# Optimization experiments

Hardware: AMD Instinct MI355X
Metric: run time of the kernel (lower is better)

The kernel has to match this reference:

```python
import jax, jax.numpy as jnp
import numpy as np

B, N, H, W = 2, 1024, 128, 128
SH_K = 27  # (sh_degree+1)^2 * 3 for sh_degree=2
L_L1, L_SSIM, L_DEPTH, L_OPAC = 0.8, 0.2, 0.5, 0.01
C0 = 0.28209479177387814


def _quat_to_rot(q):
    # q: [..., 4] (w,x,y,z) -> [..., 3, 3]
    w, x, y, z = q[..., 0], q[..., 1], q[..., 2], q[..., 3]
    R = jnp.stack([1 - 2 * (y * y + z * z), 2 * (x * y - w * z), 2 * (x * z + w * y),
                   2 * (x * y + w * z), 1 - 2 * (x * x + z * z), 2 * (y * z - w * x),
                   2 * (x * z - w * y), 2 * (y * z + w * x), 1 - 2 * (x * x + y * y)], axis=-1)
    return R.reshape(q.shape[:-1] + (3, 3))


def _ssim_window(size=7, sigma=1.5):
    coords = np.arange(size, dtype=np.float32) - size // 2
    g = np.exp(-coords ** 2 / (2 * sigma ** 2))
    g = g / g.sum()
    w2 = np.outer(g, g).astype(np.float32)
    return jnp.asarray(np.broadcast_to(w2[None, None], (3, 1, size, size)))  # OIHW, groups=3


def _dwconv(img, w):
    return jax.lax.conv_general_dilated(img, w, (1, 1), 'SAME',
                                        dimension_numbers=('NCHW', 'OIHW', 'NCHW'),
                                        feature_group_count=3)


def _ssim(img1, img2):
    C1, C2 = 0.01 ** 2, 0.03 ** 2
    w = _ssim_window()
    mu1, mu2 = _dwconv(img1, w), _dwconv(img2, w)
    s1 = _dwconv(img1 * img1, w) - mu1 ** 2
    s2 = _dwconv(img2 * img2, w) - mu2 ** 2
    s12 = _dwconv(img1 * img2, w) - mu1 * mu2
    return jnp.mean((2 * mu1 * mu2 + C1) * (2 * s12 + C2) /
                    ((mu1 ** 2 + mu2 ** 2 + C1) * (s1 + s2 + C2)))


def _render(gaussians, intrinsics):
    means = gaussians[:, :, :3]
    scales = gaussians[:, :, 3:6]
    rots = gaussians[:, :, 6:10]
    opac = gaussians[:, :, 10]        # [B,N]
    sh = gaussians[:, :, 11:]
    fx = intrinsics[:, 0, 0][:, None]
    fy = intrinsics[:, 1, 1][:, None]
    cx = intrinsics[:, 0, 2][:, None]
    cy = intrinsics[:, 1, 2][:, None]
    z = jnp.maximum(means[:, :, 2], 1e-4)
    px = fx * means[:, :, 0] / z + cx
    py = fy * means[:, :, 1] / z + cy
    # ---- 2D covariance (EWA) ----
    R = _quat_to_rot(rots)                               # [B,N,3,3]
    RS = R * scales[:, :, None, :]                        # R @ diag(s)
    cov3d = RS @ jnp.swapaxes(RS, -1, -2)
    zc = jnp.maximum(means[:, :, 2], 1e-6)
    zsq = zc * zc
    J = jnp.zeros(means.shape[:2] + (2, 3), means.dtype)
    J = J.at[:, :, 0, 0].set(fx / zc)
    J = J.at[:, :, 0, 2].set(-fx * means[:, :, 0] / zsq)
    J = J.at[:, :, 1, 1].set(fy / zc)
    J = J.at[:, :, 1, 2].set(-fy * means[:, :, 1] / zsq)
    cov2d = J @ cov3d @ jnp.swapaxes(J, -1, -2) + 0.3 * jnp.eye(2, dtype=means.dtype)
    det = jnp.maximum(cov2d[:, :, 0, 0] * cov2d[:, :, 1, 1] -
                      cov2d[:, :, 0, 1] * cov2d[:, :, 1, 0], 1e-8)
    inv00 = cov2d[:, :, 1, 1] / det
    inv11 = cov2d[:, :, 0, 0] / det
    inv01 = -cov2d[:, :, 0, 1] / det
    colors = jnp.clip(sh[:, :, :3] * C0 + 0.5, 0.0, 1.0)  # [B,N,3]
    # ---- dense per-pixel splatting ----
    gy = jnp.arange(H, dtype=means.dtype)
    gx = jnp.arange(W, dtype=means.dtype)
    dx = gx[None, None, None, :] - px[:, :, None, None]   # [B,N,1,W] -> bcast [B,N,H,W]
    dy = gy[None, None, :, None] - py[:, :, None, None]
    power = -0.5 * (inv00[:, :, None, None] * dx * dx +
                    2.0 * inv01[:, :, None, None] * dx * dy +
                    inv11[:, :, None, None] * dy * dy)
    alpha = jnp.exp(jnp.clip(power, -10.0, 0.0)) * opac[:, :, None, None]
    alpha = jnp.minimum(alpha, 0.99)
    # ---- depth sort + front-to-back compositing ----
    order = jnp.argsort(z, axis=1)
    alpha_s = jnp.take_along_axis(alpha, order[:, :, None, None], axis=1)
    colors_s = jnp.take_along_axis(colors, order[:, :, None], axis=1)
    depth_s = jnp.take_along_axis(z, order, axis=1)
    cp = jnp.cumprod(1.0 - alpha_s, axis=1)
    Tr = jnp.concatenate([jnp.ones_like(alpha_s[:, :1]), cp[:, :-1]], axis=1)
    weights = Tr * alpha_s                               # [B,N,H,W]
    rgb = jnp.clip(jnp.einsum('bnhw,bnc->bchw', weights, colors_s), 0.0, 1.0)
    depth = jnp.sum(weights * depth_s[:, :, None, None], axis=1, keepdims=True)
    return rgb, depth


def setup_inputs() -> dict:
    key = jax.random.key(0)
    k = jax.random.split(key, 8)
    xy = jax.random.normal(k[0], (B, N, 2)) * 1.0
    zc = jax.random.uniform(k[1], (B, N, 1), minval=0.5, maxval=4.0)
    scales = jax.random.uniform(k[2], (B, N, 3), minval=0.01, maxval=0.1)
    q = jax.random.normal(k[3], (B, N, 4))
    q = q / jnp.linalg.norm(q, axis=-1, keepdims=True)
    opac = jax.nn.sigmoid(jax.random.normal(k[4], (B, N, 1)))
    sh = jax.random.normal(k[5], (B, N, SH_K)) * 0.3
    gaussians = jnp.concatenate([xy, zc, scales, q, opac, sh], axis=-1)  # [B,N,38]
    intr = jnp.tile(jnp.array([[120.0, 0.0, 64.0], [0.0, 120.0, 64.0], [0.0, 0.0, 1.0]],
                              dtype=jnp.float32)[None], (B, 1, 1))
    target_rgb = jax.random.uniform(k[6], (B, 3, H, W))
    target_depth = jax.random.uniform(k[7], (B, 1, H, W), minval=0.5, maxval=4.0)
    return {'gaussians': gaussians, 'intrinsics': intr,
            'target_rgb': target_rgb, 'target_depth': target_depth}


def reference(gaussians, intrinsics, target_rgb, target_depth):
    rgb, depth = _render(gaussians, intrinsics)
    l1_rgb = jnp.mean(jnp.abs(rgb - target_rgb))
    ssim_val = _ssim(rgb, target_rgb)
    l1_depth = jnp.mean(jnp.abs(depth - target_depth))
    o = jnp.clip(gaussians[:, :, 10:11], 1e-6, 1.0 - 1e-6)
    opacity_reg = jnp.mean(-(o * jnp.log(o) + (1.0 - o) * jnp.log(1.0 - o)))
    loss = (L_L1 * l1_rgb + L_SSIM * (1.0 - ssim_val) +
            L_DEPTH * l1_depth + L_OPAC * opacity_reg)
    return loss
```

## Files before the change

kernel.cpp:

```cpp
#include <hip/hip_runtime.h>

#define NB 2
#define NG 1024
#define HEIGHT 128
#define WIDTH 128
#define HW (HEIGHT * WIDTH)
#define E10 4.5399931e-05f

#define REC_U 0
#define REC_S 32768
#define Z_U   65536
#define PFX   67584
#define TCNT  83984
#define TLIST 84496
#define RGBOF 346640
#define P_ENT 444944
#define P_L1D 444952
#define P_SSS 445464
#define P_SSL 445848

__device__ inline float blk_reduce(float v, float* sh) {
    for (int off = 32; off > 0; off >>= 1) v += __shfl_down(v, off, 64);
    int lane = threadIdx.x & 63;
    int w = threadIdx.x >> 6;
    __syncthreads();
    if (lane == 0) sh[w] = v;
    __syncthreads();
    float s = 0.f;
    if (threadIdx.x == 0) {
        int nw = (blockDim.x + 63) >> 6;
        for (int i = 0; i < nw; i++) s += sh[i];
    }
    return s;
}

__global__ __launch_bounds__(256) void k_pre(const float* __restrict__ g,
                                             const float* __restrict__ intr,
                                             float* __restrict__ ws) {
    __shared__ float sh[8];
    int idx = blockIdx.x * 256 + threadIdx.x;
    int b = idx >> 10;
    const float* row = g + (size_t)idx * 38;
    float mx = row[0], my = row[1], mz = row[2];
    float sx = row[3], sy = row[4], sz = row[5];
    float qw = row[6], qx = row[7], qy = row[8], qz = row[9];
    float op = row[10];
    float sh0 = row[11], sh1 = row[12], sh2 = row[13];
    float fx = intr[b * 9 + 0], fy = intr[b * 9 + 4];
    float cx = intr[b * 9 + 2], cy = intr[b * 9 + 5];

    float z = fmaxf(mz, 1e-4f);
    float px = fx * mx / z + cx;
    float py = fy * my / z + cy;

    float r00 = 1.f - 2.f * (qy * qy + qz * qz), r01 = 2.f * (qx * qy - qw * qz), r02 = 2.f * (qx * qz + qw * qy);
    float r10 = 2.f * (qx * qy + qw * qz), r11 = 1.f - 2.f * (qx * qx + qz * qz), r12 = 2.f * (qy * qz - qw * qx);
    float r20 = 2.f * (qx * qz - qw * qy), r21 = 2.f * (qy * qz + qw * qx), r22 = 1.f - 2.f * (qx * qx + qy * qy);
    float a00 = r00 * sx, a01 = r01 * sy, a02 = r02 * sz;
    float a10 = r10 * sx, a11 = r11 * sy, a12 = r12 * sz;
    float a20 = r20 * sx, a21 = r21 * sy, a22 = r22 * sz;
    float m00 = a00 * a00 + a01 * a01 + a02 * a02;
    float m01 = a00 * a10 + a01 * a11 + a02 * a12;
    float m02 = a00 * a20 + a01 * a21 + a02 * a22;
    float m11 = a10 * a10 + a11 * a11 + a12 * a12;
    float m12 = a10 * a20 + a11 * a21 + a12 * a22;
    float m22 = a20 * a20 + a21 * a21 + a22 * a22;

    float zc = fmaxf(mz, 1e-6f);
    float aJ = fx / zc, bJ = -fx * mx / (zc * zc);
    float cJ = fy / zc, dJ = -fy * my / (zc * zc);
    float c00 = aJ * aJ * m00 + 2.f * aJ * bJ * m02 + bJ * bJ * m22 + 0.3f;
    float c01 = cJ * (aJ * m01 + bJ * m12) + dJ * (aJ * m02 + bJ * m22);
    float c11 = cJ * cJ * m11 + 2.f * cJ * dJ * m12 + dJ * dJ * m22 + 0.3f;
    float det = fmaxf(c00 * c11 - c01 * c01, 1e-8f);
    float i00 = c11 / det;
    float i11 = c00 / det;
    float i01 = -c01 / det;

    const float C0c = 0.28209479177387814f;
    float col0 = fminf(fmaxf(sh0 * C0c + 0.5f, 0.f), 1.f);
    float col1 = fminf(fmaxf(sh1 * C0c + 0.5f, 0.f), 1.f);
    float col2 = fminf(fmaxf(sh2 * C0c + 0.5f, 0.f), 1.f);

    float hx = sqrtf(20.f * c00);
    float hy = sqrtf(20.f * c11);

    float* rec = ws + REC_U + (size_t)idx * 16;
    rec[0] = px; rec[1] = py; rec[2] = hx; rec[3] = hy;
    rec[4] = i00; rec[5] = i01; rec[6] = i11; rec[7] = op;
    rec[8] = col0; rec[9] = col1; rec[10] = col2; rec[11] = z;
    rec[12] = E10 * op; rec[13] = 0.f; rec[14] = 0.f; rec[15] = 0.f;
    ws[Z_U + idx] = z;

    float o = fminf(fmaxf(op, 1e-6f), 1.f - 1e-6f);
    float ent = -(o * logf(o) + (1.f - o) * logf(1.f - o));
    float s = blk_reduce(ent, sh);
    if (threadIdx.x == 0) ws[P_ENT + blockIdx.x] = s;
}

__global__ __launch_bounds__(256) void k_rank(float* __restrict__ ws) {
    __shared__ float zs[NG];
    __shared__ int sp[256];
    int bid = blockIdx.x;
    int b = bid >> 4;
    int grp = bid & 15;
    int tid = threadIdx.x;
    const float* zb = ws + Z_U + (b << 10);
    ((float4*)zs)[tid] = ((const float4*)zb)[tid];
    __syncthreads();
    int il = (grp << 6) + (tid & 63);
    int jq = tid >> 6;
    float zi = zs[il];
    int rank = 0;
    int j0 = jq << 8;
#pragma unroll 4
    for (int j = j0; j < j0 + 256; j += 4) {
        float4 zq = *(const float4*)(zs + j);
        rank += (zq.x < zi) || (zq.x == zi && (j + 0) < il);
        rank += (zq.y < zi) || (zq.y == zi && (j + 1) < il);
        rank += (zq.z < zi) || (zq.z == zi && (j + 2) < il);
        rank += (zq.w < zi) || (zq.w == zi && (j + 3) < il);
    }
    sp[tid] = rank;
    __syncthreads();
    if (tid < 64) {
        int r = sp[tid] + sp[tid + 64] + sp[tid + 128] + sp[tid + 192];
        int gi = (b << 10) + il;
        const float4* src = (const float4*)(ws + REC_U + (size_t)gi * 16);
        float4 r0 = src[0], r1 = src[1], r2 = src[2], r3 = src[3];
        float4* dst = (float4*)(ws + REC_S + (size_t)((b << 10) + r) * 16);
        dst[0] = r0; dst[1] = r1; dst[2] = r2; dst[3] = r3;
    }
}

__global__ __launch_bounds__(1024) void k_scan(float* __restrict__ ws) {
    __shared__ float st[NG], sur[NG], sug[NG], sub_[NG], sud[NG];
    int b = blockIdx.x;
    int k = threadIdx.x;
    const float* r = ws + REC_S + (size_t)((b << 10) + k) * 16;
    float4 f1 = ((const float4*)r)[1];
    float4 f2 = ((const float4*)r)[2];
    float a10 = E10 * f1.w;
    st[k] = 1.f - a10;
    sur[k] = a10 * f2.x; sug[k] = a10 * f2.y; sub_[k] = a10 * f2.z; sud[k] = a10 * f2.w;
    __syncthreads();
    for (int off = 1; off < NG; off <<= 1) {
        float tl = 1.f, url = 0.f, ugl = 0.f, ubl = 0.f, udl = 0.f;
        if (k >= off) {
            tl = st[k - off]; url = sur[k - off]; ugl = sug[k - off];
            ubl = sub_[k - off]; udl = sud[k - off];
        }
        __syncthreads();
        if (k >= off) {
            sur[k] = url + tl * sur[k];
            sug[k] = ugl + tl * sug[k];
            sub_[k] = ubl + tl * sub_[k];
            sud[k] = udl + tl * sud[k];
            st[k] = tl * st[k];
        }
        __syncthreads();
    }
    float* P = ws + PFX + (size_t)b * 8200;
    ((float4*)(P + (size_t)(k + 1) * 8))[0] = make_float4(st[k], sur[k], sug[k], sub_[k]);
    P[(size_t)(k + 1) * 8 + 4] = sud[k];
    if (k == 0) {
        ((float4*)P)[0] = make_float4(1.f, 0.f, 0.f, 0.f);
        P[4] = 0.f;
    }
}

__global__ __launch_bounds__(256) void k_bin(float* __restrict__ ws) {
    __shared__ int sc[256];
    int blk = blockIdx.x;
    int b = blk >> 8;
    int t = blk & 255;
    float x0f = (float)((t & 15) * 8), x1f = x0f + 7.f;
    float y0f = (float)((t >> 4) * 8), y1f = y0f + 7.f;
    int tid = threadIdx.x;
    int r0 = tid * 4;
    int pred = 0;
#pragma unroll
    for (int j = 0; j < 4; j++) {
        float4 bb = ((const float4*)(ws + REC_S + (size_t)((b << 10) + r0 + j) * 16))[0];
        bool ov = (bb.x + bb.z >= x0f) && (bb.x - bb.z <= x1f) &&
                  (bb.y + bb.w >= y0f) && (bb.y - bb.w <= y1f);
        pred |= (int)ov << j;
    }
    int cnt = __popc(pred);
    sc[tid] = cnt;
    __syncthreads();
    for (int off = 1; off < 256; off <<= 1) {
        int v = 0;
        if (tid >= off) v = sc[tid - off];
        __syncthreads();
        sc[tid] += v;
        __syncthreads();
    }
    unsigned short* list = (unsigned short*)(ws + TLIST) + (size_t)blk * 1024;
    int pos = sc[tid] - cnt;
#pragma unroll
    for (int j = 0; j < 4; j++)
        if (pred & (1 << j)) list[pos++] = (unsigned short)(r0 + j);
    if (tid == 255) ((int*)(ws + TCNT))[blk] = sc[255];
}

__global__ __launch_bounds__(1024, 8) void k_render(const float* __restrict__ tgt_d,
                                                    float* __restrict__ ws) {
    __shared__ float comb[5][1024];
    int tid = threadIdx.x;
    int lane = tid & 63;
    int wv = tid >> 6;
    int blk = blockIdx.x;
    int b = blk >> 8;
    int t = blk & 255;
    int x0 = (t & 15) * 8, y0 = (t >> 4) * 8;
    int x = x0 + (lane & 7), y = y0 + (lane >> 3);
    float xf = (float)x, yf = (float)y;

    int cnt = ((const int*)(ws + TCNT))[blk];
    const unsigned short* list = (const unsigned short*)(ws + TLIST) + (size_t)blk * 1024;
    const float* P = ws + PFX + (size_t)b * 8200;
    const float* recs = ws + REC_S + (size_t)(b << 10) * 16;

    int m = (cnt + 15) >> 4;
    int p0 = wv * m; if (p0 > cnt) p0 = cnt;
    int p1 = p0 + m; if (p1 > cnt) p1 = cnt;
    int s0 = (p0 == 0) ? 0 : (int)list[p0 - 1] + 1;

    float4 Pa = *(const float4*)(P + (size_t)s0 * 8);
    float Pud = P[(size_t)s0 * 8 + 4];
    float inv0 = 1.f / Pa.x;
    float Pur = Pa.y, Pug = Pa.z, Pub = Pa.w;

    float tau = 1.f, cr = 0.f, cg = 0.f, cb = 0.f, cd = 0.f;
    for (int p = p0; p < p1; p++) {
        int r = (int)list[p];
        float4 Qa = *(const float4*)(P + (size_t)r * 8);
        float Qud = P[(size_t)r * 8 + 4];
        const float* rec = recs + (size_t)r * 16;
        float4 g0 = ((const float4*)rec)[0];
        float4 g1 = ((const float4*)rec)[1];
        float4 g2 = ((const float4*)rec)[2];
        float kap = tau * inv0;
        cr += kap * (Qa.y - Pur);
        cg += kap * (Qa.z - Pug);
        cb += kap * (Qa.w - Pub);
        cd += kap * (Qud - Pud);
        float dx = xf - g0.x, dy = yf - g0.y;
        float q = g1.x * dx * dx + 2.f * g1.y * dx * dy + g1.z * dy * dy;
        float pw = fminf(fmaxf(-0.5f * q, -10.f), 0.f);
        float a = fminf(__expf(pw) * g1.w, 0.99f);
        float w = kap * Qa.x * a;
        cr += w * g2.x; cg += w * g2.y; cb += w * g2.z; cd += w * g2.w;
        float a10 = E10 * g1.w;
        tau *= (1.f - a) * (1.f + a10 * (1.f + a10));
        float s = Qa.x * a10;
        Pur = Qa.y + s * g2.x;
        Pug = Qa.z + s * g2.y;
        Pub = Qa.w + s * g2.z;
        Pud = Qud + s * g2.w;
    }
    int e0 = (wv == 15) ? NG : ((p1 == 0) ? 0 : (int)list[p1 - 1] + 1);
    float4 Ea = *(const float4*)(P + (size_t)e0 * 8);
    float Eud = P[(size_t)e0 * 8 + 4];
    float kapf = tau * inv0;
    cr += kapf * (Ea.y - Pur);
    cg += kapf * (Ea.z - Pug);
    cb += kapf * (Ea.w - Pub);
    cd += kapf * (Eud - Pud);
    float T = tau * Ea.x * inv0;

    comb[0][tid] = T;
    comb[1][tid] = cr;
    comb[2][tid] = cg;
    comb[3][tid] = cb;
    comb[4][tid] = cd;
    __syncthreads();

    if (tid < 64) {
        float T0 = comb[0][tid], r0 = comb[1][tid], g0 = comb[2][tid];
        float b0 = comb[3][tid], d0 = comb[4][tid];
#pragma unroll
        for (int sgi = 1; sgi < 16; sgi++) {
            int j = sgi * 64 + tid;
            r0 += T0 * comb[1][j];
            g0 += T0 * comb[2][j];
            b0 += T0 * comb[3][j];
            d0 += T0 * comb[4][j];
            T0 *= comb[0][j];
        }
        r0 = fminf(fmaxf(r0, 0.f), 1.f);
        g0 = fminf(fmaxf(g0, 0.f), 1.f);
        b0 = fminf(fmaxf(b0, 0.f), 1.f);
        float* rgb = ws + RGBOF;
        rgb[((b * 3 + 0) * HEIGHT + y) * WIDTH + x] = r0;
        rgb[((b * 3 + 1) * HEIGHT + y) * WIDTH + x] = g0;
        rgb[((b * 3 + 2) * HEIGHT + y) * WIDTH + x] = b0;
        float l1d = fabsf(d0 - tgt_d[(b * HEIGHT + y) * WIDTH + x]);
        for (int off = 32; off > 0; off >>= 1) l1d += __shfl_down(l1d, off, 64);
        if (tid == 0) ws[P_L1D + blk] = l1d;
    }
}

__global__ __launch_bounds__(256) void k_ssim(const float* __restrict__ tgt_rgb,
                                              float* __restrict__ ws) {
    __shared__ float sh[8];
    int idx = blockIdx.x * 256 + threadIdx.x;
    const float* img1 = ws + RGBOF;
    int bc = idx >> 14;
    int pix = idx & (HW - 1);
    int y = pix >> 7, x = pix & 127;

    float gg[7];
    float gs = 0.f;
#pragma unroll
    for (int i = 0; i < 7; i++) {
        float c = (float)(i - 3);
        gg[i] = __expf(-c * c / 4.5f);
        gs += gg[i];
    }
#pragma unroll
    for (int i = 0; i < 7; i++) gg[i] /= gs;

    float mu1 = 0.f, mu2 = 0.f, s11 = 0.f, s22 = 0.f, s12 = 0.f;
    int plane = bc * HW;
#pragma unroll
    for (int dy = -3; dy <= 3; dy++) {
        int yy = y + dy;
#pragma unroll
        for (int dx = -3; dx <= 3; dx++) {
            int xx = x + dx;
            float w = gg[dy + 3] * gg[dx + 3];
            float i1 = 0.f, i2 = 0.f;
            if (yy >= 0 && yy < HEIGHT && xx >= 0 && xx < WIDTH) {
                int o = plane + yy * WIDTH + xx;
                i1 = img1[o];
                i2 = tgt_rgb[o];
            }
            mu1 += w * i1;
            mu2 += w * i2;
            s11 += w * i1 * i1;
            s22 += w * i2 * i2;
            s12 += w * i1 * i2;
        }
    }
    float v1 = s11 - mu1 * mu1;
    float v2 = s22 - mu2 * mu2;
    float cv = s12 - mu1 * mu2;
    const float C1 = 1e-4f, C2 = 9e-4f;
    float ssim = ((2.f * mu1 * mu2 + C1) * (2.f * cv + C2)) /
                 ((mu1 * mu1 + mu2 * mu2 + C1) * (v1 + v2 + C2));
    float l1 = fabsf(img1[idx] - tgt_rgb[idx]);

    float s_ssim = blk_reduce(ssim, sh);
    float s_l1 = blk_reduce(l1, sh);
    if (threadIdx.x == 0) {
        ws[P_SSS + blockIdx.x] = s_ssim;
        ws[P_SSL + blockIdx.x] = s_l1;
    }
}

__global__ __launch_bounds__(256) void k_final(const float* __restrict__ ws_c,
                                               float* __restrict__ out) {
    __shared__ float sh[8];
    float e = 0.f, d = 0.f, ss = 0.f, sl = 0.f;
    for (int i = threadIdx.x; i < 512; i += 256) d += ws_c[P_L1D + i];
    for (int i = threadIdx.x; i < 384; i += 256) { ss += ws_c[P_SSS + i]; sl += ws_c[P_SSL + i]; }
    if (threadIdx.x < 8) e = ws_c[P_ENT + threadIdx.x];
    float rd_ = blk_reduce(d, sh);
    float rss = blk_reduce(ss, sh);
    float rsl = blk_reduce(sl, sh);
    float re = blk_reduce(e, sh);
    if (threadIdx.x == 0) {
        float l1r = rsl / (float)(NB * 3 * HW);
        float ssim = rss / (float)(NB * 3 * HW);
        float l1d = rd_ / (float)(NB * HW);
        float opa = re / (float)(NB * NG);
        out[0] = 0.8f * l1r + 0.2f * (1.f - ssim) + 0.5f * l1d + 0.01f * opa;
    }
}

extern "C" void kernel_launch(void* const* d_in, const int* in_sizes, int n_in,
                              void* d_out, int out_size, void* d_ws, size_t ws_size,
                              hipStream_t stream) {
    const float* g = (const float*)d_in[0];
    const float* intr = (const float*)d_in[1];
    const float* trgb = (const float*)d_in[2];
    const float* tdep = (const float*)d_in[3];
    float* ws = (float*)d_ws;
    float* out = (float*)d_out;

    hipLaunchKernelGGL(k_pre, dim3(8), dim3(256), 0, stream, g, intr, ws);
    hipLaunchKernelGGL(k_rank, dim3(32), dim3(256), 0, stream, ws);
    hipLaunchKernelGGL(k_scan, dim3(NB), dim3(1024), 0, stream, ws);
    hipLaunchKernelGGL(k_bin, dim3(NB * 256), dim3(256), 0, stream, ws);
    hipLaunchKernelGGL(k_render, dim3(NB * 256), dim3(1024), 0, stream, tdep, ws);
    hipLaunchKernelGGL(k_ssim, dim3((NB * 3 * HW) / 256), dim3(256), 0, stream, trgb, ws);
    hipLaunchKernelGGL(k_final, dim3(1), dim3(256), 0, stream, ws, out);
}
```

Baseline: 97.65 us.

## Fuse all loss stages into one cooperative kernel with grid-wide syncs

```diff
diff --git a/kernel.cpp b/kernel.cpp
--- a/kernel.cpp
+++ b/kernel.cpp
@@ -1,4 +1,7 @@
 #include <hip/hip_runtime.h>
+#include <hip/hip_cooperative_groups.h>
+
+namespace cg = cooperative_groups;
 
 #define NB 2
 #define NG 1024
@@ -10,373 +13,385 @@
 #define REC_U 0
 #define REC_S 32768
 #define Z_U   65536
-#define PFX   67584
-#define TCNT  83984
-#define TLIST 84496
-#define RGBOF 346640
-#define P_ENT 444944
-#define P_L1D 444952
-#define P_SSS 445464
-#define P_SSL 445848
-
-__device__ inline float blk_reduce(float v, float* sh) {
-    for (int off = 32; off > 0; off >>= 1) v += __shfl_down(v, off, 64);
-    int lane = threadIdx.x & 63;
-    int w = threadIdx.x >> 6;
-    __syncthreads();
-    if (lane == 0) sh[w] = v;
-    __syncthreads();
-    float s = 0.f;
-    if (threadIdx.x == 0) {
-        int nw = (blockDim.x + 63) >> 6;
-        for (int i = 0; i < nw; i++) s += sh[i];
-    }
-    return s;
-}
-
-__global__ __launch_bounds__(256) void k_pre(const float* __restrict__ g,
-                                             const float* __restrict__ intr,
-                                             float* __restrict__ ws) {
-    __shared__ float sh[8];
-    int idx = blockIdx.x * 256 + threadIdx.x;
-    int b = idx >> 10;
-    const float* row = g + (size_t)idx * 38;
-    float mx = row[0], my = row[1], mz = row[2];
-    float sx = row[3], sy = row[4], sz = row[5];
-    float qw = row[6], qx = row[7], qy = row[8], qz = row[9];
-    float op = row[10];
-    float sh0 = row[11], sh1 = row[12], sh2 = row[13];
-    float fx = intr[b * 9 + 0], fy = intr[b * 9 + 4];
-    float cx = intr[b * 9 + 2], cy = intr[b * 9 + 5];
-
-    float z = fmaxf(mz, 1e-4f);
-    float px = fx * mx / z + cx;
-    float py = fy * my / z + cy;
-
-    float r00 = 1.f - 2.f * (qy * qy + qz * qz), r01 = 2.f * (qx * qy - qw * qz), r02 = 2.f * (qx * qz + qw * qy);
-    float r10 = 2.f * (qx * qy + qw * qz), r11 = 1.f - 2.f * (qx * qx + qz * qz), r12 = 2.f * (qy * qz - qw * qx);
-    float r20 = 2.f * (qx * qz - qw * qy), r21 = 2.f * (qy * qz + qw * qx), r22 = 1.f - 2.f * (qx * qx + qy * qy);
-    float a00 = r00 * sx, a01 = r01 * sy, a02 = r02 * sz;
-    float a10 = r10 * sx, a11 = r11 * sy, a12 = r12 * sz;
-    float a20 = r20 * sx, a21 = r21 * sy, a22 = r22 * sz;
-    float m00 = a00 * a00 + a01 * a01 + a02 * a02;
-    float m01 = a00 * a10 + a01 * a11 + a02 * a12;
-    float m02 = a00 * a20 + a01 * a21 + a02 * a22;
-    float m11 = a10 * a10 + a11 * a11 + a12 * a12;
-    float m12 = a10 * a20 + a11 * a21 + a12 * a22;
-    float m22 = a20 * a20 + a21 * a21 + a22 * a22;
-
-    float zc = fmaxf(mz, 1e-6f);
-    float aJ = fx / zc, bJ = -fx * mx / (zc * zc);
-    float cJ = fy / zc, dJ = -fy * my / (zc * zc);
-    float c00 = aJ * aJ * m00 + 2.f * aJ * bJ * m02 + bJ * bJ * m22 + 0.3f;
-    float c01 = cJ * (aJ * m01 + bJ * m12) + dJ * (aJ * m02 + bJ * m22);
-    float c11 = cJ * cJ * m11 + 2.f * cJ * dJ * m12 + dJ * dJ * m22 + 0.3f;
-    float det = fmaxf(c00 * c11 - c01 * c01, 1e-8f);
-    float i00 = c11 / det;
-    float i11 = c00 / det;
-    float i01 = -c01 / det;
-
-    const float C0c = 0.28209479177387814f;
-    float col0 = fminf(fmaxf(sh0 * C0c + 0.5f, 0.f), 1.f);
-    float col1 = fminf(fmaxf(sh1 * C0c + 0.5f, 0.f), 1.f);
-    float col2 = fminf(fmaxf(sh2 * C0c + 0.5f, 0.f), 1.f);
-
-    float hx = sqrtf(20.f * c00);
-    float hy = sqrtf(20.f * c11);
-
-    float* rec = ws + REC_U + (size_t)idx * 16;
-    rec[0] = px; rec[1] = py; rec[2] = hx; rec[3] = hy;
-    rec[4] = i00; rec[5] = i01; rec[6] = i11; rec[7] = op;
-    rec[8] = col0; rec[9] = col1; rec[10] = col2; rec[11] = z;
-    rec[12] = E10 * op; rec[13] = 0.f; rec[14] = 0.f; rec[15] = 0.f;
-    ws[Z_U + idx] = z;
-
-    float o = fminf(fmaxf(op, 1e-6f), 1.f - 1e-6f);
-    float ent = -(o * logf(o) + (1.f - o) * logf(1.f - o));
-    float s = blk_reduce(ent, sh);
-    if (threadIdx.x == 0) ws[P_ENT + blockIdx.x] = s;
-}
-
-__global__ __launch_bounds__(256) void k_rank(float* __restrict__ ws) {
-    __shared__ float zs[NG];
-    __shared__ int sp[256];
-    int bid = blockIdx.x;
-    int b = bid >> 4;
-    int grp = bid & 15;
-    int tid = threadIdx.x;
-    const float* zb = ws + Z_U + (b << 10);
-    ((float4*)zs)[tid] = ((const float4*)zb)[tid];
-    __syncthreads();
-    int il = (grp << 6) + (tid & 63);
-    int jq = tid >> 6;
-    float zi = zs[il];
-    int rank = 0;
-    int j0 = jq << 8;
+#define BBOX  67584
+#define PFX   75776
+#define PFX_STRIDE 8200
+#define TCNT  92192
+#define TLIST 92704
+#define RGBOF 354848
+#define P_ENT 453152
+#define P_L1D 453184
+#define P_SSS 453696
+#define P_SSL 453952
+
+__global__ __launch_bounds__(1024, 4) void k_mega(
+    const float* __restrict__ g, const float* __restrict__ intr,
+    const float* __restrict__ trgb, const float* __restrict__ tgt_d,
+    float* __restrict__ ws, float* __restrict__ out)
+{
+    __shared__ float smem[5120];
+    cg::grid_group grid = cg::this_grid();
+    const int tid = threadIdx.x;
+    const int bid = blockIdx.x;
+    const int lane = tid & 63;
+    const int wv = tid >> 6;
+
+    if (bid < 2) {
+        int idx = bid * 1024 + tid;
+        int b = bid;
+        const float* row = g + (size_t)idx * 38;
+        float mx = row[0], my = row[1], mz = row[2];
+        float sx = row[3], sy = row[4], sz = row[5];
+        float qw = row[6], qx = row[7], qy = row[8], qz = row[9];
+        float op = row[10];
+        float sh0 = row[11], sh1 = row[12], sh2 = row[13];
+        float fx = intr[b * 9 + 0], fy = intr[b * 9 + 4];
+        float cx = intr[b * 9 + 2], cy = intr[b * 9 + 5];
+
+        float z = fmaxf(mz, 1e-4f);
+        float px = fx * mx / z + cx;
+        float py = fy * my / z + cy;
+
+        float r00 = 1.f - 2.f * (qy * qy + qz * qz), r01 = 2.f * (qx * qy - qw * qz), r02 = 2.f * (qx * qz + qw * qy);
+        float r10 = 2.f * (qx * qy + qw * qz), r11 = 1.f - 2.f * (qx * qx + qz * qz), r12 = 2.f * (qy * qz - qw * qx);
+        float r20 = 2.f * (qx * qz - qw * qy), r21 = 2.f * (qy * qz + qw * qx), r22 = 1.f - 2.f * (qx * qx + qy * qy);
+        float a00 = r00 * sx, a01 = r01 * sy, a02 = r02 * sz;
+        float a10 = r10 * sx, a11 = r11 * sy, a12 = r12 * sz;
+        float a20 = r20 * sx, a21 = r21 * sy, a22 = r22 * sz;
+        float m00 = a00 * a00 + a01 * a01 + a02 * a02;
+        float m01 = a00 * a10 + a01 * a11 + a02 * a12;
+        float m02 = a00 * a20 + a01 * a21 + a02 * a22;
+        float m11 = a10 * a10 + a11 * a11 + a12 * a12;
+        float m12 = a10 * a20 + a11 * a21 + a12 * a22;
+        float m22 = a20 * a20 + a21 * a21 + a22 * a22;
+
+        float zc = fmaxf(mz, 1e-6f);
+        float aJ = fx / zc, bJ = -fx * mx / (zc * zc);
+        float cJ = fy / zc, dJ = -fy * my / (zc * zc);
+        float c00 = aJ * aJ * m00 + 2.f * aJ * bJ * m02 + bJ * bJ * m22 + 0.3f;
+        float c01 = cJ * (aJ * m01 + bJ * m12) + dJ * (aJ * m02 + bJ * m22);
+        float c11 = cJ * cJ * m11 + 2.f * cJ * dJ * m12 + dJ * dJ * m22 + 0.3f;
+        float det = fmaxf(c00 * c11 - c01 * c01, 1e-8f);
+        float i00 = c11 / det;
+        float i11 = c00 / det;
+        float i01 = -c01 / det;
+
+        const float C0c = 0.28209479177387814f;
+        float col0 = fminf(fmaxf(sh0 * C0c + 0.5f, 0.f), 1.f);
+        float col1 = fminf(fmaxf(sh1 * C0c + 0.5f, 0.f), 1.f);
+        float col2 = fminf(fmaxf(sh2 * C0c + 0.5f, 0.f), 1.f);
+
+        float hx = sqrtf(20.f * c00);
+        float hy = sqrtf(20.f * c11);
+
+        float* rec = ws + REC_U + (size_t)idx * 16;
+        rec[0] = px; rec[1] = py; rec[2] = hx; rec[3] = hy;
+        rec[4] = i00; rec[5] = i01; rec[6] = i11; rec[7] = op;
+        rec[8] = col0; rec[9] = col1; rec[10] = col2; rec[11] = z;
+        rec[12] = E10 * op; rec[13] = 0.f; rec[14] = 0.f; rec[15] = 0.f;
+        ws[Z_U + idx] = z;
+
+        float o = fminf(fmaxf(op, 1e-6f), 1.f - 1e-6f);
+        float ent = -(o * logf(o) + (1.f - o) * logf(1.f - o));
+        for (int off = 32; off > 0; off >>= 1) ent += __shfl_down(ent, off, 64);
+        if (lane == 0) ws[P_ENT + (bid << 4) + wv] = ent;
+    }
+    grid.sync();
+
+    if (bid < 8) {
+        int b = bid >> 2, part = bid & 3;
+        float* zs = smem;
+        int* spi = (int*)(smem + 1024);
+        if (tid < 256) ((float4*)zs)[tid] = ((const float4*)(ws + Z_U + (b << 10)))[tid];
+        __syncthreads();
+        int c = tid & 255, jq = tid >> 8;
+        int il = part * 256 + c;
+        float zi = zs[il];
+        int rank = 0;
+        int j0 = jq << 8;
 #pragma unroll 4
-    for (int j = j0; j < j0 + 256; j += 4) {
-        float4 zq = *(const float4*)(zs + j);
-        rank += (zq.x < zi) || (zq.x == zi && (j + 0) < il);
-        rank += (zq.y < zi) || (zq.y == zi && (j + 1) < il);
-        rank += (zq.z < zi) || (zq.z == zi && (j + 2) < il);
-        rank += (zq.w < zi) || (zq.w == zi && (j + 3) < il);
-    }
-    sp[tid] = rank;
-    __syncthreads();
-    if (tid < 64) {
-        int r = sp[tid] + sp[tid + 64] + sp[tid + 128] + sp[tid + 192];
-        int gi = (b << 10) + il;
-        const float4* src = (const float4*)(ws + REC_U + (size_t)gi * 16);
-        float4 r0 = src[0], r1 = src[1], r2 = src[2], r3 = src[3];
-        float4* dst = (float4*)(ws + REC_S + (size_t)((b << 10) + r) * 16);
-        dst[0] = r0; dst[1] = r1; dst[2] = r2; dst[3] = r3;
-    }
-}
-
-__global__ __launch_bounds__(1024) void k_scan(float* __restrict__ ws) {
-    __shared__ float st[NG], sur[NG], sug[NG], sub_[NG], sud[NG];
-    int b = blockIdx.x;
-    int k = threadIdx.x;
-    const float* r = ws + REC_S + (size_t)((b << 10) + k) * 16;
-    float4 f1 = ((const float4*)r)[1];
-    float4 f2 = ((const float4*)r)[2];
-    float a10 = E10 * f1.w;
-    st[k] = 1.f - a10;
-    sur[k] = a10 * f2.x; sug[k] = a10 * f2.y; sub_[k] = a10 * f2.z; sud[k] = a10 * f2.w;
-    __syncthreads();
-    for (int off = 1; off < NG; off <<= 1) {
-        float tl = 1.f, url = 0.f, ugl = 0.f, ubl = 0.f, udl = 0.f;
-        if (k >= off) {
-            tl = st[k - off]; url = sur[k - off]; ugl = sug[k - off];
-            ubl = sub_[k - off]; udl = sud[k - off];
-        }
-        __syncthreads();
-        if (k >= off) {
-            sur[k] = url + tl * sur[k];
-            sug[k] = ugl + tl * sug[k];
-            sub_[k] = ubl + tl * sub_[k];
-            sud[k] = udl + tl * sud[k];
-            st[k] = tl * st[k];
-        }
-        __syncthreads();
-    }
-    float* P = ws + PFX + (size_t)b * 8200;
-    ((float4*)(P + (size_t)(k + 1) * 8))[0] = make_float4(st[k], sur[k], sug[k], sub_[k]);
-    P[(size_t)(k + 1) * 8 + 4] = sud[k];
-    if (k == 0) {
-        ((float4*)P)[0] = make_float4(1.f, 0.f, 0.f, 0.f);
-        P[4] = 0.f;
-    }
-}
-
-__global__ __launch_bounds__(256) void k_bin(float* __restrict__ ws) {
-    __shared__ int sc[256];
-    int blk = blockIdx.x;
-    int b = blk >> 8;
-    int t = blk & 255;
-    float x0f = (float)((t & 15) * 8), x1f = x0f + 7.f;
-    float y0f = (float)((t >> 4) * 8), y1f = y0f + 7.f;
-    int tid = threadIdx.x;
-    int r0 = tid * 4;
-    int pred = 0;
-#pragma unroll
-    for (int j = 0; j < 4; j++) {
-        float4 bb = ((const float4*)(ws + REC_S + (size_t)((b << 10) + r0 + j) * 16))[0];
-        bool ov = (bb.x + bb.z >= x0f) && (bb.x - bb.z <= x1f) &&
-                  (bb.y + bb.w >= y0f) && (bb.y - bb.w <= y1f);
-        pred |= (int)ov << j;
-    }
-    int cnt = __popc(pred);
-    sc[tid] = cnt;
-    __syncthreads();
-    for (int off = 1; off < 256; off <<= 1) {
-        int v = 0;
-        if (tid >= off) v = sc[tid - off];
-        __syncthreads();
-        sc[tid] += v;
-        __syncthreads();
-    }
-    unsigned short* list = (unsigned short*)(ws + TLIST) + (size_t)blk * 1024;
-    int pos = sc[tid] - cnt;
-#pragma unroll
-    for (int j = 0; j < 4; j++)
-        if (pred & (1 << j)) list[pos++] = (unsigned short)(r0 + j);
-    if (tid == 255) ((int*)(ws + TCNT))[blk] = sc[255];
-}
-
-__global__ __launch_bounds__(1024, 8) void k_render(const float* __restrict__ tgt_d,
-                                                    float* __restrict__ ws) {
-    __shared__ float comb[5][1024];
-    int tid = threadIdx.x;
-    int lane = tid & 63;
-    int wv = tid >> 6;
-    int blk = blockIdx.x;
-    int b = blk >> 8;
-    int t = blk & 255;
-    int x0 = (t & 15) * 8, y0 = (t >> 4) * 8;
-    int x = x0 + (lane & 7), y = y0 + (lane >> 3);
-    float xf = (float)x, yf = (float)y;
-
-    int cnt = ((const int*)(ws + TCNT))[blk];
-    const unsigned short* list = (const unsigned short*)(ws + TLIST) + (size_t)blk * 1024;
-    const float* P = ws + PFX + (size_t)b * 8200;
-    const float* recs = ws + REC_S + (size_t)(b << 10) * 16;
-
-    int m = (cnt + 15) >> 4;
-    int p0 = wv * m; if (p0 > cnt) p0 = cnt;
-    int p1 = p0 + m; if (p1 > cnt) p1 = cnt;
-    int s0 = (p0 == 0) ? 0 : (int)list[p0 - 1] + 1;
-
-    float4 Pa = *(const float4*)(P + (size_t)s0 * 8);
-    float Pud = P[(size_t)s0 * 8 + 4];
-    float inv0 = 1.f / Pa.x;
-    float Pur = Pa.y, Pug = Pa.z, Pub = Pa.w;
-
-    float tau = 1.f, cr = 0.f, cg = 0.f, cb = 0.f, cd = 0.f;
-    for (int p = p0; p < p1; p++) {
-        int r = (int)list[p];
-        float4 Qa = *(const float4*)(P + (size_t)r * 8);
-        float Qud = P[(size_t)r * 8 + 4];
-        const float* rec = recs + (size_t)r * 16;
-        float4 g0 = ((const float4*)rec)[0];
-        float4 g1 = ((const float4*)rec)[1];
-        float4 g2 = ((const float4*)rec)[2];
-        float kap = tau * inv0;
-        cr += kap * (Qa.y - Pur);
-        cg += kap * (Qa.z - Pug);
-        cb += kap * (Qa.w - Pub);
-        cd += kap * (Qud - Pud);
-        float dx = xf - g0.x, dy = yf - g0.y;
-        float q = g1.x * dx * dx + 2.f * g1.y * dx * dy + g1.z * dy * dy;
-        float pw = fminf(fmaxf(-0.5f * q, -10.f), 0.f);
-        float a = fminf(__expf(pw) * g1.w, 0.99f);
-        float w = kap * Qa.x * a;
-        cr += w * g2.x; cg += w * g2.y; cb += w * g2.z; cd += w * g2.w;
-        float a10 = E10 * g1.w;
-        tau *= (1.f - a) * (1.f + a10 * (1.f + a10));
-        float s = Qa.x * a10;
-        Pur = Qa.y + s * g2.x;
-        Pug = Qa.z + s * g2.y;
-        Pub = Qa.w + s * g2.z;
-        Pud = Qud + s * g2.w;
-    }
-    int e0 = (wv == 15) ? NG : ((p1 == 0) ? 0 : (int)list[p1 - 1] + 1);
-    float4 Ea = *(const float4*)(P + (size_t)e0 * 8);
-    float Eud = P[(size_t)e0 * 8 + 4];
-    float kapf = tau * inv0;
-    cr += kapf * (Ea.y - Pur);
-    cg += kapf * (Ea.z - Pug);
-    cb += kapf * (Ea.w - Pub);
-    cd += kapf * (Eud - Pud);
-    float T = tau * Ea.x * inv0;
-
-    comb[0][tid] = T;
-    comb[1][tid] = cr;
-    comb[2][tid] = cg;
-    comb[3][tid] = cb;
-    comb[4][tid] = cd;
-    __syncthreads();
-
-    if (tid < 64) {
-        float T0 = comb[0][tid], r0 = comb[1][tid], g0 = comb[2][tid];
-        float b0 = comb[3][tid], d0 = comb[4][tid];
-#pragma unroll
-        for (int sgi = 1; sgi < 16; sgi++) {
-            int j = sgi * 64 + tid;
-            r0 += T0 * comb[1][j];
-            g0 += T0 * comb[2][j];
-            b0 += T0 * comb[3][j];
-            d0 += T0 * comb[4][j];
-            T0 *= comb[0][j];
-        }
-        r0 = fminf(fmaxf(r0, 0.f), 1.f);
-        g0 = fminf(fmaxf(g0, 0.f), 1.f);
-        b0 = fminf(fmaxf(b0, 0.f), 1.f);
-        float* rgb = ws + RGBOF;
-        rgb[((b * 3 + 0) * HEIGHT + y) * WIDTH + x] = r0;
-        rgb[((b * 3 + 1) * HEIGHT + y) * WIDTH + x] = g0;
-        rgb[((b * 3 + 2) * HEIGHT + y) * WIDTH + x] = b0;
-        float l1d = fabsf(d0 - tgt_d[(b * HEIGHT + y) * WIDTH + x]);
-        for (int off = 32; off > 0; off >>= 1) l1d += __shfl_down(l1d, off, 64);
-        if (tid == 0) ws[P_L1D + blk] = l1d;
-    }
-}
-
-__global__ __launch_bounds__(256) void k_ssim(const float* __restrict__ tgt_rgb,
-                                              float* __restrict__ ws) {
-    __shared__ float sh[8];
-    int idx = blockIdx.x * 256 + threadIdx.x;
-    const float* img1 = ws + RGBOF;
-    int bc = idx >> 14;
-    int pix = idx & (HW - 1);
-    int y = pix >> 7, x = pix & 127;
-
-    float gg[7];
-    float gs = 0.f;
-#pragma unroll
-    for (int i = 0; i < 7; i++) {
-        float c = (float)(i - 3);
-        gg[i] = __expf(-c * c / 4.5f);
-        gs += gg[i];
-    }
-#pragma unroll
-    for (int i = 0; i < 7; i++) gg[i] /= gs;
-
-    float mu1 = 0.f, mu2 = 0.f, s11 = 0.f, s22 = 0.f, s12 = 0.f;
-    int plane = bc * HW;
-#pragma unroll
-    for (int dy = -3; dy <= 3; dy++) {
-        int yy = y + dy;
-#pragma unroll
-        for (int dx = -3; dx <= 3; dx++) {
-            int xx = x + dx;
-            float w = gg[dy + 3] * gg[dx + 3];
-            float i1 = 0.f, i2 = 0.f;
-            if (yy >= 0 && yy < HEIGHT && xx >= 0 && xx < WIDTH) {
-                int o = plane + yy * WIDTH + xx;
-                i1 = img1[o];
-                i2 = tgt_rgb[o];
-            }
-            mu1 += w * i1;
-            mu2 += w * i2;
-            s11 += w * i1 * i1;
-            s22 += w * i2 * i2;
-            s12 += w * i1 * i2;
-        }
-    }
-    float v1 = s11 - mu1 * mu1;
-    float v2 = s22 - mu2 * mu2;
-    float cv = s12 - mu1 * mu2;
-    const float C1 = 1e-4f, C2 = 9e-4f;
-    float ssim = ((2.f * mu1 * mu2 + C1) * (2.f * cv + C2)) /
-                 ((mu1 * mu1 + mu2 * mu2 + C1) * (v1 + v2 + C2));
-    float l1 = fabsf(img1[idx] - tgt_rgb[idx]);
-
-    float s_ssim = blk_reduce(ssim, sh);
-    float s_l1 = blk_reduce(l1, sh);
-    if (threadIdx.x == 0) {
-        ws[P_SSS + blockIdx.x] = s_ssim;
-        ws[P_SSL + blockIdx.x] = s_l1;
-    }
-}
-
-__global__ __launch_bounds__(256) void k_final(const float* __restrict__ ws_c,
-                                               float* __restrict__ out) {
-    __shared__ float sh[8];
-    float e = 0.f, d = 0.f, ss = 0.f, sl = 0.f;
-    for (int i = threadIdx.x; i < 512; i += 256) d += ws_c[P_L1D + i];
-    for (int i = threadIdx.x; i < 384; i += 256) { ss += ws_c[P_SSS + i]; sl += ws_c[P_SSL + i]; }
-    if (threadIdx.x < 8) e = ws_c[P_ENT + threadIdx.x];
-    float rd_ = blk_reduce(d, sh);
-    float rss = blk_reduce(ss, sh);
-    float rsl = blk_reduce(sl, sh);
-    float re = blk_reduce(e, sh);
-    if (threadIdx.x == 0) {
-        float l1r = rsl / (float)(NB * 3 * HW);
-        float ssim = rss / (float)(NB * 3 * HW);
-        float l1d = rd_ / (float)(NB * HW);
-        float opa = re / (float)(NB * NG);
-        out[0] = 0.8f * l1r + 0.2f * (1.f - ssim) + 0.5f * l1d + 0.01f * opa;
+        for (int j = j0; j < j0 + 256; j += 4) {
+            float4 zq = *(const float4*)(zs + j);
+            rank += (zq.x < zi) || (zq.x == zi && (j + 0) < il);
+            rank += (zq.y < zi) || (zq.y == zi && (j + 1) < il);
+            rank += (zq.z < zi) || (zq.z == zi && (j + 2) < il);
+            rank += (zq.w < zi) || (zq.w == zi && (j + 3) < il);
+        }
+        spi[tid] = rank;
+        __syncthreads();
+        if (tid < 256) {
+            int r = spi[tid] + spi[tid + 256] + spi[tid + 512] + spi[tid + 768];
+            int gi = (b << 10) + part * 256 + tid;
+            const float4* src = (const float4*)(ws + REC_U + (size_t)gi * 16);
+            float4 r0 = src[0], r1 = src[1], r2 = src[2], r3 = src[3];
+            float4* dst = (float4*)(ws + REC_S + (size_t)((b << 10) + r) * 16);
+            dst[0] = r0; dst[1] = r1; dst[2] = r2; dst[3] = r3;
+            ((float4*)(ws + BBOX))[(b << 10) + r] = r0;
+        }
+    }
+    grid.sync();
+
+    if (bid < 2) {
+        int b = bid;
+        const float* rec = ws + REC_S + (size_t)((b << 10) + tid) * 16;
+        float4 f1 = ((const float4*)rec)[1];
+        float4 f2 = ((const float4*)rec)[2];
+        float a10 = E10 * f1.w;
+        float t = 1.f - a10;
+        float ur = a10 * f2.x, ug = a10 * f2.y, ub = a10 * f2.z, ud = a10 * f2.w;
+#pragma unroll
+        for (int off = 1; off < 64; off <<= 1) {
+            float pt = __shfl_up(t, off, 64);
+            float pr = __shfl_up(ur, off, 64);
+            float pg = __shfl_up(ug, off, 64);
+            float pb = __shfl_up(ub, off, 64);
+            float pd = __shfl_up(ud, off, 64);
+            if (lane >= off) {
+                ur = pr + pt * ur; ug = pg + pt * ug;
+                ub = pb + pt * ub; ud = pd + pt * ud;
+                t = pt * t;
+            }
+        }
+        if (lane == 63) {
+            smem[wv * 5 + 0] = t;  smem[wv * 5 + 1] = ur; smem[wv * 5 + 2] = ug;
+            smem[wv * 5 + 3] = ub; smem[wv * 5 + 4] = ud;
+        }
+        __syncthreads();
+        float Pt = 1.f, Pur = 0.f, Pug = 0.f, Pub = 0.f, Pud = 0.f;
+        for (int i = 0; i < wv; i++) {
+            float at = smem[i * 5], ar = smem[i * 5 + 1], ag = smem[i * 5 + 2];
+            float ab = smem[i * 5 + 3], ad = smem[i * 5 + 4];
+            Pur = Pur + Pt * ar; Pug = Pug + Pt * ag;
+            Pub = Pub + Pt * ab; Pud = Pud + Pt * ad;
+            Pt = Pt * at;
+        }
+        float gt = Pt * t;
+        float gur = Pur + Pt * ur, gug = Pug + Pt * ug;
+        float gub = Pub + Pt * ub, gud = Pud + Pt * ud;
+        float* P = ws + PFX + (size_t)b * PFX_STRIDE;
+        ((float4*)(P + (size_t)(tid + 1) * 8))[0] = make_float4(gt, gur, gug, gub);
+        P[(size_t)(tid + 1) * 8 + 4] = gud;
+        if (tid == 0) {
+            ((float4*)P)[0] = make_float4(1.f, 0.f, 0.f, 0.f);
+            P[4] = 0.f;
+        }
+    }
+    {
+        int* wcnt = (int*)smem;
+        for (int t2 = 0; t2 < 2; t2++) {
+            __syncthreads();
+            int blk_t = bid + t2 * 256;
+            int b = blk_t >> 8, tt = blk_t & 255;
+            float x0f = (float)((tt & 15) * 8), x1f = x0f + 7.f;
+            float y0f = (float)((tt >> 4) * 8), y1f = y0f + 7.f;
+            float4 bb = ((const float4*)(ws + BBOX))[(b << 10) + tid];
+            bool ov = (bb.x + bb.z >= x0f) && (bb.x - bb.z <= x1f) &&
+                      (bb.y + bb.w >= y0f) && (bb.y - bb.w <= y1f);
+            unsigned long long mask = __ballot(ov);
+            int loff = __popcll(mask & ((1ull << lane) - 1ull));
+            if (lane == 0) wcnt[wv] = (int)__popcll(mask);
+            __syncthreads();
+            int woff = 0, totc = 0;
+#pragma unroll
+            for (int i = 0; i < 16; i++) {
+                int ci = wcnt[i];
+                woff += (i < wv) ? ci : 0;
+                totc += ci;
+            }
+            unsigned short* list = (unsigned short*)(ws + TLIST) + (size_t)blk_t * 1024;
+            if (ov) list[woff + loff] = (unsigned short)tid;
+            if (tid == 0) ((int*)(ws + TCNT))[blk_t] = totc;
+        }
+    }
+    grid.sync();
+
+    for (int t2 = 0; t2 < 2; t2++) {
+        __syncthreads();
+        int blk_t = bid + t2 * 256;
+        int b = blk_t >> 8, tt = blk_t & 255;
+        int x0 = (tt & 15) * 8, y0 = (tt >> 4) * 8;
+        int x = x0 + (lane & 7), y = y0 + (lane >> 3);
+        float xf = (float)x, yf = (float)y;
+
+        int cnt = ((const int*)(ws + TCNT))[blk_t];
+        const unsigned short* list = (const unsigned short*)(ws + TLIST) + (size_t)blk_t * 1024;
+        const float* P = ws + PFX + (size_t)b * PFX_STRIDE;
+        const float* recs = ws + REC_S + (size_t)(b << 10) * 16;
+
+        int m = (cnt + 15) >> 4;
+        int p0 = wv * m; if (p0 > cnt) p0 = cnt;
+        int p1 = p0 + m; if (p1 > cnt) p1 = cnt;
+        int s0 = (p0 == 0) ? 0 : (int)list[p0 - 1] + 1;
+
+        float4 Pa = *(const float4*)(P + (size_t)s0 * 8);
+        float Pud = P[(size_t)s0 * 8 + 4];
+        float inv0 = 1.f / Pa.x;
+        float Pur = Pa.y, Pug = Pa.z, Pub = Pa.w;
+
+        float tau = 1.f, cr = 0.f, cgn = 0.f, cb = 0.f, cd = 0.f;
+        for (int p = p0; p < p1; p++) {
+            int r = (int)list[p];
+            float4 Qa = *(const float4*)(P + (size_t)r * 8);
+            float Qud = P[(size_t)r * 8 + 4];
+            const float* rec = recs + (size_t)r * 16;
+            float4 g0 = ((const float4*)rec)[0];
+            float4 g1 = ((const float4*)rec)[1];
+            float4 g2 = ((const float4*)rec)[2];
+            float kap = tau * inv0;
+            cr += kap * (Qa.y - Pur);
+            cgn += kap * (Qa.z - Pug);
+            cb += kap * (Qa.w - Pub);
+            cd += kap * (Qud - Pud);
+            float dx = xf - g0.x, dy = yf - g0.y;
+            float q = g1.x * dx * dx + 2.f * g1.y * dx * dy + g1.z * dy * dy;
+            float pw = fminf(fmaxf(-0.5f * q, -10.f), 0.f);
+            float a = fminf(__expf(pw) * g1.w, 0.99f);
+            float w = kap * Qa.x * a;
+            cr += w * g2.x; cgn += w * g2.y; cb += w * g2.z; cd += w * g2.w;
+            float a10 = E10 * g1.w;
+            tau *= (1.f - a) * (1.f + a10 * (1.f + a10));
+            float s = Qa.x * a10;
+            Pur = Qa.y + s * g2.x;
+            Pug = Qa.z + s * g2.y;
+            Pub = Qa.w + s * g2.z;
+            Pud = Qud + s * g2.w;
+        }
+        int e0 = (wv == 15) ? NG : ((p1 == 0) ? 0 : (int)list[p1 - 1] + 1);
+        float4 Ea = *(const float4*)(P + (size_t)e0 * 8);
+        float Eud = P[(size_t)e0 * 8 + 4];
+        float kapf = tau * inv0;
+        cr += kapf * (Ea.y - Pur);
+        cgn += kapf * (Ea.z - Pug);
+        cb += kapf * (Ea.w - Pub);
+        cd += kapf * (Eud - Pud);
+        float T = tau * Ea.x * inv0;
+
+        smem[0 * 1024 + tid] = T;
+        smem[1 * 1024 + tid] = cr;
+        smem[2 * 1024 + tid] = cgn;
+        smem[3 * 1024 + tid] = cb;
+        smem[4 * 1024 + tid] = cd;
+        __syncthreads();
+
+        if (tid < 64) {
+            float T0 = smem[tid], r0 = smem[1024 + tid], g0 = smem[2048 + tid];
+            float b0 = smem[3072 + tid], d0 = smem[4096 + tid];
+#pragma unroll
+            for (int sgi = 1; sgi < 16; sgi++) {
+                int j = sgi * 64 + tid;
+                r0 += T0 * smem[1024 + j];
+                g0 += T0 * smem[2048 + j];
+                b0 += T0 * smem[3072 + j];
+                d0 += T0 * smem[4096 + j];
+                T0 *= smem[j];
+            }
+            r0 = fminf(fmaxf(r0, 0.f), 1.f);
+            g0 = fminf(fmaxf(g0, 0.f), 1.f);
+            b0 = fminf(fmaxf(b0, 0.f), 1.f);
+            float* rgb = ws + RGBOF;
+            rgb[((b * 3 + 0) * HEIGHT + y) * WIDTH + x] = r0;
+            rgb[((b * 3 + 1) * HEIGHT + y) * WIDTH + x] = g0;
+            rgb[((b * 3 + 2) * HEIGHT + y) * WIDTH + x] = b0;
+            float l1d = fabsf(d0 - tgt_d[(b * HEIGHT + y) * WIDTH + x]);
+            for (int off = 32; off > 0; off >>= 1) l1d += __shfl_down(l1d, off, 64);
+            if (tid == 0) ws[P_L1D + blk_t] = l1d;
+        }
+    }
+    grid.sync();
+
+    {
+        float ssim = 0.f, l1 = 0.f;
+        if (tid < 384) {
+            int idx = bid * 384 + tid;
+            const float* img1 = ws + RGBOF;
+            int bc = idx >> 14;
+            int pix = idx & (HW - 1);
+            int y = pix >> 7, x = pix & 127;
+
+            float gg[7];
+            float gs = 0.f;
+#pragma unroll
+            for (int i = 0; i < 7; i++) {
+                float c = (float)(i - 3);
+                gg[i] = __expf(-c * c / 4.5f);
+                gs += gg[i];
+            }
+#pragma unroll
+            for (int i = 0; i < 7; i++) gg[i] /= gs;
+
+            float mu1 = 0.f, mu2 = 0.f, s11 = 0.f, s22 = 0.f, s12 = 0.f;
+            int plane = bc * HW;
+#pragma unroll
+            for (int dy = -3; dy <= 3; dy++) {
+                int yy = y + dy;
+#pragma unroll
+                for (int dx = -3; dx <= 3; dx++) {
+                    int xx = x + dx;
+                    float w = gg[dy + 3] * gg[dx + 3];
+                    float i1 = 0.f, i2 = 0.f;
+                    if (yy >= 0 && yy < HEIGHT && xx >= 0 && xx < WIDTH) {
+                        int o = plane + yy * WIDTH + xx;
+                        i1 = img1[o];
+                        i2 = trgb[o];
+                    }
+                    mu1 += w * i1;
+                    mu2 += w * i2;
+                    s11 += w * i1 * i1;
+                    s22 += w * i2 * i2;
+                    s12 += w * i1 * i2;
+                }
+            }
+            float v1 = s11 - mu1 * mu1;
+            float v2 = s22 - mu2 * mu2;
+            float cv = s12 - mu1 * mu2;
+            const float C1 = 1e-4f, C2 = 9e-4f;
+            ssim = ((2.f * mu1 * mu2 + C1) * (2.f * cv + C2)) /
+                   ((mu1 * mu1 + mu2 * mu2 + C1) * (v1 + v2 + C2));
+            l1 = fabsf(img1[idx] - trgb[idx]);
+        }
+        for (int off = 32; off > 0; off >>= 1) {
+            ssim += __shfl_down(ssim, off, 64);
+            l1 += __shfl_down(l1, off, 64);
+        }
+        if (lane == 0) { smem[wv] = ssim; smem[16 + wv] = l1; }
+        __syncthreads();
+        if (tid == 0) {
+            float ss = 0.f, sl = 0.f;
+#pragma unroll
+            for (int i = 0; i < 16; i++) { ss += smem[i]; sl += smem[16 + i]; }
+            ws[P_SSS + bid] = ss;
+            ws[P_SSL + bid] = sl;
+        }
+    }
+    grid.sync();
+
+    if (bid == 0) {
+        float d = 0.f, ss = 0.f, sl = 0.f, e = 0.f;
+        if (tid < 512) d = ws[P_L1D + tid];
+        if (tid < 256) { ss = ws[P_SSS + tid]; sl = ws[P_SSL + tid]; }
+        if (tid < 32) e = ws[P_ENT + tid];
+        for (int off = 32; off > 0; off >>= 1) {
+            d += __shfl_down(d, off, 64);
+            ss += __shfl_down(ss, off, 64);
+            sl += __shfl_down(sl, off, 64);
+            e += __shfl_down(e, off, 64);
+        }
+        if (lane == 0) {
+            smem[wv] = d; smem[16 + wv] = ss; smem[32 + wv] = sl; smem[48 + wv] = e;
+        }
+        __syncthreads();
+        if (tid == 0) {
+            float rd = 0.f, rss = 0.f, rsl = 0.f, re = 0.f;
+#pragma unroll
+            for (int i = 0; i < 16; i++) {
+                rd += smem[i]; rss += smem[16 + i]; rsl += smem[32 + i]; re += smem[48 + i];
+            }
+            float l1r = rsl / (float)(NB * 3 * HW);
+            float ssim = rss / (float)(NB * 3 * HW);
+            float l1d = rd / (float)(NB * HW);
+            float opa = re / (float)(NB * NG);
+            out[0] = 0.8f * l1r + 0.2f * (1.f - ssim) + 0.5f * l1d + 0.01f * opa;
+        }
     }
 }
 
@@ -390,11 +405,7 @@
     float* ws = (float*)d_ws;
     float* out = (float*)d_out;
 
-    hipLaunchKernelGGL(k_pre, dim3(8), dim3(256), 0, stream, g, intr, ws);
-    hipLaunchKernelGGL(k_rank, dim3(32), dim3(256), 0, stream, ws);
-    hipLaunchKernelGGL(k_scan, dim3(NB), dim3(1024), 0, stream, ws);
-    hipLaunchKernelGGL(k_bin, dim3(NB * 256), dim3(256), 0, stream, ws);
-    hipLaunchKernelGGL(k_render, dim3(NB * 256), dim3(1024), 0, stream, tdep, ws);
-    hipLaunchKernelGGL(k_ssim, dim3((NB * 3 * HW) / 256), dim3(256), 0, stream, trgb, ws);
-    hipLaunchKernelGGL(k_final, dim3(1), dim3(256), 0, stream, ws, out);
+    void* args[] = {(void*)&g, (void*)&intr, (void*)&trgb, (void*)&tdep,
+                    (void*)&ws, (void*)&out};
+    hipLaunchCooperativeKernel((void*)k_mega, dim3(256), dim3(1024), args, 0, stream);
 }
```

Result: slower. 228.7 us (+134.2%).
